# Kernel optimization log

Measured on AMD Instinct MI355X. Metric: run time of the kernel, lower is better.

## Reference

```python
import jax, jax.numpy as jnp
import numpy as np
import math

B, S, D, H = 8, 1024, 256, 8
HD = D // H  # head size = 32


def setup_inputs() -> dict:
    key = jax.random.key(0)
    ks = jax.random.split(key, 12)
    inp = {
        "query": jax.random.normal(ks[0], (B, S, D), jnp.float32),
        "key": jax.random.normal(ks[1], (B, S, D), jnp.float32),
        "value": jax.random.normal(ks[2], (B, S, D), jnp.float32),
        "rel": jax.random.uniform(ks[3], (B, S, S), jnp.float32),
        "timestamp": jax.random.normal(ks[4], (B, S, S), jnp.float32),
        "l1": jax.random.uniform(ks[5], (1,), jnp.float32),
        "l2": jax.random.uniform(ks[6], (1,), jnp.float32),
        # projection weights (nn.Linear: y = x @ W.T + b)
        "Wq": jax.random.normal(ks[7], (D, D), jnp.float32) / math.sqrt(D),
        "bq": jnp.zeros((D,), jnp.float32),
        "Wk": jax.random.normal(ks[8], (D, D), jnp.float32) / math.sqrt(D),
        "bk": jnp.zeros((D,), jnp.float32),
        "Wv": jax.random.normal(ks[9], (D, D), jnp.float32) / math.sqrt(D),
        "bv": jnp.zeros((D,), jnp.float32),
    }
    return inp


def reference(query, key, value, rel, timestamp, l1, l2, Wq, bq, Wk, bk, Wv, bv):
    b, s, d = query.shape
    h, hd = H, HD

    def proj(x, W, bias):
        # [b,s,d] -> [b,h,s,hd]
        return (x @ W.T + bias).reshape(b, s, h, hd).transpose(0, 2, 1, 3)

    q = proj(query, Wq, bq)
    k = proj(key, Wk, bk)
    v = proj(value, Wv, bv)

    # causal future mask: True above the diagonal (future positions)
    mask = jnp.triu(jnp.ones((s, s), dtype=bool), k=1)[None, None]  # [1,1,s,s]

    # relation attention: rel * mask, zeros -> -10000, softmax
    relm = rel[:, None] * mask.astype(rel.dtype)  # broadcast over heads [b,1->h,s,s]
    rel_attn = jax.nn.softmax(jnp.where(relm == 0, jnp.float32(-10000.0), relm), axis=-1)

    # scaled dot-product scores with causal mask
    scores = jnp.einsum('bhqd,bhkd->bhqk', q, k) / math.sqrt(hd)
    scores = jnp.where(mask, jnp.float32(-1e9), scores)
    prob_attn = jax.nn.softmax(scores, axis=-1)

    # time-decay attention: exp(-|t|), masked to -inf (use -1e30 for grad safety)
    ts = jnp.where(mask, jnp.float32(-1e30), jnp.exp(-jnp.abs(timestamp[:, None])))
    time_attn = jax.nn.softmax(ts, axis=-1)

    # blend (time_include=True, qrelation_include=True)
    prob = (1.0 - l2) * prob_attn + l2 * time_attn
    prob = (1.0 - l1) * prob + l1 * rel_attn

    out = jnp.einsum('bhqk,bhkd->bhqd', prob, v)
    out = out.transpose(0, 2, 1, 3).reshape(b, s, d)
    return out
```

## Files before the change

### kernel.cpp

```cpp
#include <hip/hip_runtime.h>
#include <math.h>

constexpr int B = 8, S = 1024, D = 256, H = 8, HD = 32;

typedef __attribute__((ext_vector_type(8))) short bf16x8;
typedef __attribute__((ext_vector_type(16))) float f32x16;
typedef __attribute__((ext_vector_type(2)))  int  int2v;

__device__ __forceinline__ uint cvtpk(float a, float b) {
    uint r;
    asm("v_cvt_pk_bf16_f32 %0, %1, %2" : "=v"(r) : "v"(a), "v"(b));
    return r;
}
__device__ __forceinline__ float xswap32f(float v, int hi) {
    int2v t = __builtin_amdgcn_permlane32_swap(__float_as_int(v), __float_as_int(v), false, false);
    return __int_as_float(hi ? t[0] : t[1]);
}

__global__ __launch_bounds__(512, 4) void proj_mfma(
    const float* __restrict__ query, const float* __restrict__ key_,
    const float* __restrict__ value,
    const float* __restrict__ Wq, const float* __restrict__ Wk,
    const float* __restrict__ Wv,
    const float* __restrict__ bq, const float* __restrict__ bk,
    const float* __restrict__ bv, float qscale,
    ushort* __restrict__ qbuf, ushort* __restrict__ kbuf,
    ushort* __restrict__ vtbuf, float* __restrict__ cpart)
{
    __shared__ ushort xf[8192];
    __shared__ float bias_lds[256];

    const int m = blockIdx.y;
    const int tid = threadIdx.x;
    const int w = tid >> 6, lane = tid & 63;
    const int l31 = lane & 31, hi = lane >> 5;
    const int h = w;

    const float* xsrc = (m == 0) ? query : (m == 1) ? key_ : value;
    const float* Wsrc = (m == 0) ? Wq : (m == 1) ? Wk : Wv;
    const float* bsrc = (m == 0) ? bq : (m == 1) ? bk : bv;
    ushort* yb = (m == 0) ? qbuf : (m == 1) ? kbuf : vtbuf;
    const float wscale = (m == 0) ? qscale : 1.0f;

    if (tid < 256) bias_lds[tid] = bsrc[tid] * wscale;

    bf16x8 wf[16];
    {
        const float* wrow = Wsrc + ((size_t)(h * 32 + l31)) * 256 + hi * 8;
        #pragma unroll
        for (int kc = 0; kc < 16; ++kc) {
            float4 a = *(const float4*)(wrow + kc * 16);
            float4 b = *(const float4*)(wrow + kc * 16 + 4);
            uint4 p;
            p.x = cvtpk(a.x * wscale, a.y * wscale);
            p.y = cvtpk(a.z * wscale, a.w * wscale);
            p.z = cvtpk(b.x * wscale, b.y * wscale);
            p.w = cvtpk(b.z * wscale, b.w * wscale);
            wf[kc] = __builtin_bit_cast(bf16x8, p);
        }
    }

    const int sst = tid & 31, skc = tid >> 5;
    float cpacc = 0.f;

    for (int it = 0; it < 2; ++it) {
        const int stile = blockIdx.x * 2 + it;
        const int b_ = stile >> 5, t32 = stile & 31;

        __syncthreads();
        {
            const float* xrow = xsrc + ((size_t)(stile * 32 + sst)) * 256 + skc * 16;
            float4 a0 = *(const float4*)(xrow + 0);
            float4 a1 = *(const float4*)(xrow + 4);
            float4 a2 = *(const float4*)(xrow + 8);
            float4 a3 = *(const float4*)(xrow + 12);
            uint2 w01 = { cvtpk(a0.x, a0.y), cvtpk(a0.z, a0.w) };
            uint2 w23 = { cvtpk(a1.x, a1.y), cvtpk(a1.z, a1.w) };
            uint2 w45 = { cvtpk(a2.x, a2.y), cvtpk(a2.z, a2.w) };
            uint2 w67 = { cvtpk(a3.x, a3.y), cvtpk(a3.z, a3.w) };
            ushort* base = xf + skc * 512 + sst * 4;
            *(uint2*)(base +   0) = w01;
            *(uint2*)(base + 128) = w23;
            *(uint2*)(base + 256) = w45;
            *(uint2*)(base + 384) = w67;
        }
        __syncthreads();

        f32x16 acc;
        #pragma unroll
        for (int r = 0; r < 16; ++r) acc[r] = 0.f;
        #pragma unroll
        for (int kc = 0; kc < 16; ++kc) {
            const ushort* rb = xf + kc * 512 + hi * 256 + l31 * 4;
            uint2 lo = *(const uint2*)rb;
            uint2 hj = *(const uint2*)(rb + 128);
            uint4 xw = { lo.x, lo.y, hj.x, hj.y };
            bf16x8 xfrag = __builtin_bit_cast(bf16x8, xw);
            if (m < 2)
                acc = __builtin_amdgcn_mfma_f32_32x32x16_bf16(wf[kc], xfrag, acc, 0, 0, 0);
            else
                acc = __builtin_amdgcn_mfma_f32_32x32x16_bf16(xfrag, wf[kc], acc, 0, 0, 0);
        }

        if (m < 2) {
            #pragma unroll
            for (int r = 0; r < 16; ++r)
                acc[r] += bias_lds[h * 32 + (r & 3) + 8 * (r >> 2) + 4 * hi];
        } else {
            const float bl = bias_lds[h * 32 + l31];
            #pragma unroll
            for (int r = 0; r < 16; ++r) acc[r] += bl;
            float cp = 0.f;
            #pragma unroll
            for (int r = 0; r < 16; ++r) cp += acc[r];
            cp += __shfl_xor(cp, 32);
            cpacc += cp;
        }

        uint wa0 = cvtpk(acc[0], acc[1]),   wa1 = cvtpk(acc[2], acc[3]);
        uint wb0 = cvtpk(acc[4], acc[5]),   wb1 = cvtpk(acc[6], acc[7]);
        uint wa2 = cvtpk(acc[8], acc[9]),   wa3 = cvtpk(acc[10], acc[11]);
        uint wb2 = cvtpk(acc[12], acc[13]), wb3 = cvtpk(acc[14], acc[15]);
        int2v s0 = __builtin_amdgcn_permlane32_swap((int)wa0, (int)wb0, false, false);
        int2v s1 = __builtin_amdgcn_permlane32_swap((int)wa1, (int)wb1, false, false);
        int2v s2 = __builtin_amdgcn_permlane32_swap((int)wa2, (int)wb2, false, false);
        int2v s3 = __builtin_amdgcn_permlane32_swap((int)wa3, (int)wb3, false, false);
        uint4 p0 = { (uint)s0[0], (uint)s1[0], (uint)s0[1], (uint)s1[1] };
        uint4 p1 = { (uint)s2[0], (uint)s3[0], (uint)s2[1], (uint)s3[1] };
        ushort* dst = yb + (((size_t)b_ * H + h) * 32 + t32) * 1024 + hi * 256 + l31 * 8;
        *(uint4*)dst = p0;
        *(uint4*)(dst + 512) = p1;
    }
    if (m == 2 && hi == 0)
        cpart[blockIdx.x * D + h * 32 + l31] = cpacc;
}

__global__ __launch_bounds__(512, 4) void timerel_mfma(
    const float* __restrict__ ts, const float* __restrict__ rel,
    const ushort* __restrict__ vtb, const float* __restrict__ cpart,
    const float* __restrict__ l1p, const float* __restrict__ l2p,
    float* __restrict__ out)
{
    __shared__ ushort wlds[32][1032];
    __shared__ float nuni[32];

    const int b  = blockIdx.y;
    const int i0 = blockIdx.x * 32;
    const int w = threadIdx.x >> 6, lane = threadIdx.x & 63;
    const int l31 = lane & 31, hi = lane >> 5;
    const float l1 = l1p[0], l2 = l2p[0];

    for (int r = 0; r < 4; ++r) {
        const int row = w * 4 + r;
        const int i = i0 + row;
        const float* tsrow  = ts  + ((size_t)b * S + i) * S;
        const float* relrow = rel + ((size_t)b * S + i) * S;

        float wv[4][4];
        float stp = 0.f, srp = 0.f;
        #pragma unroll
        for (int q = 0; q < 4; ++q) {
            const int jb = q * 256 + lane * 4;
            if (q * 256 + 255 <= i) {
                float4 t4 = *(const float4*)(tsrow + jb);
                const float te[4] = { t4.x, t4.y, t4.z, t4.w };
                #pragma unroll
                for (int e = 0; e < 4; ++e) {
                    float v = __expf(__expf(-fabsf(te[e])));
                    stp += v; wv[q][e] = v;
                }
            } else if (q * 256 > i) {
                float4 r4 = *(const float4*)(relrow + jb);
                const float re[4] = { r4.x, r4.y, r4.z, r4.w };
                #pragma unroll
                for (int e = 0; e < 4; ++e) {
                    float v = (re[e] != 0.f) ? __expf(re[e]) : 0.f;
                    srp += v; wv[q][e] = v;
                }
            } else {
                float4 t4 = *(const float4*)(tsrow + jb);
                float4 r4 = *(const float4*)(relrow + jb);
                const float te[4] = { t4.x, t4.y, t4.z, t4.w };
                const float re[4] = { r4.x, r4.y, r4.z, r4.w };
                #pragma unroll
                for (int e = 0; e < 4; ++e) {
                    float v;
                    if (jb + e <= i) { v = __expf(__expf(-fabsf(te[e]))); stp += v; }
                    else             { v = (re[e] != 0.f) ? __expf(re[e]) : 0.f; srp += v; }
                    wv[q][e] = v;
                }
            }
        }
        #pragma unroll
        for (int off = 1; off < 64; off <<= 1) {
            stp += __shfl_xor(stp, off);
            srp += __shfl_xor(srp, off);
        }
        const float nt = (1.f - l1) * l2 / stp;
        const float nr = (srp > 0.5f) ? (l1 / srp) : 0.f;
        if (lane == 0) nuni[row] = (srp > 0.5f) ? 0.f : (l1 / (float)S);
        #pragma unroll
        for (int q = 0; q < 4; ++q) {
            const int jb = q * 256 + lane * 4;
            float a0 = wv[q][0] * ((jb     <= i) ? nt : nr);
            float a1 = wv[q][1] * ((jb + 1 <= i) ? nt : nr);
            float a2 = wv[q][2] * ((jb + 2 <= i) ? nt : nr);
            float a3 = wv[q][3] * ((jb + 3 <= i) ? nt : nr);
            uint2 pk; pk.x = cvtpk(a0, a1); pk.y = cvtpk(a2, a3);
            *(uint2*)&wlds[row][jb] = pk;
        }
    }
    __syncthreads();

    const ushort* vtbase = vtb + ((size_t)b * 8 + w) * 32768 + hi * 256 + l31 * 8;
    f32x16 acc;
    #pragma unroll
    for (int r = 0; r < 16; ++r) acc[r] = 0.f;
    #pragma unroll 4
    for (int ks = 0; ks < 64; ++ks) {
        bf16x8 afrag = *(const bf16x8*)&wlds[l31][ks * 16 + hi * 8];
        bf16x8 vf = *(const bf16x8*)(vtbase + (size_t)ks * 512);
        acc = __builtin_amdgcn_mfma_f32_32x32x16_bf16(afrag, vf, acc, 0, 0, 0);
    }

    const int d = w * 32 + l31;
    float cv = 0.f;
    if (i0 == S - 32) {
        #pragma unroll
        for (int p_ = 0; p_ < 16; ++p_)
            cv += cpart[(b * 16 + p_) * D + d];
    }
    float* obase = out + ((size_t)b * S + i0) * D + d;
    #pragma unroll
    for (int r = 0; r < 16; ++r) {
        const int row = (r & 3) + 8 * (r >> 2) + 4 * hi;
        obase[(size_t)row * D] = acc[r] + nuni[row] * cv;
    }
}

#define LOADKV(K0, K1, V0, V1, KT) do { \
    const ushort* kp_ = kbase + (size_t)(KT) * 1024; \
    const ushort* vp_ = vbase + (size_t)(KT) * 1024; \
    K0 = *(const bf16x8*)kp_;        K1 = *(const bf16x8*)(kp_ + 512); \
    V0 = *(const bf16x8*)vp_;        V1 = *(const bf16x8*)(vp_ + 512); \
} while (0)

#define TILE_COMPUTE(K0, K1, V0, V1, ISDIAG) do { \
    f32x16 stv; \
    _Pragma("unroll") for (int r = 0; r < 16; ++r) stv[r] = 0.f; \
    stv = __builtin_amdgcn_mfma_f32_32x32x16_bf16(K0, qf0, stv, 0, 0, 0); \
    stv = __builtin_amdgcn_mfma_f32_32x32x16_bf16(K1, qf1, stv, 0, 0, 0); \
    if (ISDIAG) { \
        _Pragma("unroll") for (int r = 0; r < 16; ++r) \
            if (((r & 3) + 8 * (r >> 2) + 4 * hi) > l31) stv[r] = -1e30f; \
    } \
    float p[16]; \
    _Pragma("unroll") for (int r = 0; r < 16; ++r) { p[r] = exp2f(stv[r]); lacc += p[r]; } \
    uint wa0 = cvtpk(p[0], p[1]),   wa1 = cvtpk(p[2], p[3]); \
    uint wb0 = cvtpk(p[4], p[5]),   wb1 = cvtpk(p[6], p[7]); \
    uint wa2 = cvtpk(p[8], p[9]),   wa3 = cvtpk(p[10], p[11]); \
    uint wb2 = cvtpk(p[12], p[13]), wb3 = cvtpk(p[14], p[15]); \
    int2v s0 = __builtin_amdgcn_permlane32_swap((int)wa0, (int)wb0, false, false); \
    int2v s1 = __builtin_amdgcn_permlane32_swap((int)wa1, (int)wb1, false, false); \
    int2v s2 = __builtin_amdgcn_permlane32_swap((int)wa2, (int)wb2, false, false); \
    int2v s3 = __builtin_amdgcn_permlane32_swap((int)wa3, (int)wb3, false, false); \
    uint4 pa0i = { (uint)s0[0], (uint)s1[0], (uint)s0[1], (uint)s1[1] }; \
    uint4 pa1i = { (uint)s2[0], (uint)s3[0], (uint)s2[1], (uint)s3[1] }; \
    bf16x8 pa0 = __builtin_bit_cast(bf16x8, pa0i); \
    bf16x8 pa1 = __builtin_bit_cast(bf16x8, pa1i); \
    ot = __builtin_amdgcn_mfma_f32_32x32x16_bf16(V0, pa0, ot, 0, 0, 0); \
    ot = __builtin_amdgcn_mfma_f32_32x32x16_bf16(V1, pa1, ot, 0, 0, 0); \
} while (0)

__global__ __launch_bounds__(512, 4) void flash_mfma(
    const ushort* __restrict__ qb, const ushort* __restrict__ kb,
    const ushort* __restrict__ vtb, const float* __restrict__ l1p,
    const float* __restrict__ l2p, float* __restrict__ out)
{
    __shared__ float mbuf[4][64][18];
    __shared__ float lds_t[4][32 * 33];
    const int id = blockIdx.x;
    const int halfg = id >> 8, rr_ = id & 255;
    const int qraw = rr_ >> 5;
    const int qblk = halfg ? (7 - qraw) : qraw;
    const int bh = (rr_ & 31) | (halfg << 5);
    const int b = bh >> 3, h = bh & 7;
    const int w = threadIdx.x >> 6, lane = threadIdx.x & 63;
    const int sub = w & 3, half = w >> 2;
    const int l31 = lane & 31, hi = lane >> 5;
    const int qt = qblk * 4 + sub;
    const float c_p = (1.f - l1p[0]) * (1.f - l2p[0]);

    const ushort* qp_ = qb + ((size_t)bh * 32 + qt) * 1024 + hi * 256 + l31 * 8;
    const bf16x8 qf0 = *(const bf16x8*)qp_;
    const bf16x8 qf1 = *(const bf16x8*)(qp_ + 512);
    const ushort* kbase = kb  + (size_t)bh * 32768 + hi * 256 + l31 * 8;
    const ushort* vbase = vtb + (size_t)bh * 32768 + hi * 256 + l31 * 8;

    f32x16 ot;
    #pragma unroll
    for (int r = 0; r < 16; ++r) ot[r] = 0.f;
    float lacc = 0.f;

    const int nlo = (qt + 1) >> 1;
    const int klo = half ? nlo : 0;
    const int khi = half ? qt : (nlo - 1);

    if (klo <= khi) {
        bf16x8 kA0, kA1, vA0, vA1, kB0, kB1, vB0, vB1;
        LOADKV(kA0, kA1, vA0, vA1, klo);
        int kt = klo;
        for (;;) {
            if (kt + 1 <= khi) LOADKV(kB0, kB1, vB0, vB1, kt + 1);
            TILE_COMPUTE(kA0, kA1, vA0, vA1, kt == qt);
            if (++kt > khi) break;
            if (kt + 1 <= khi) LOADKV(kA0, kA1, vA0, vA1, kt + 1);
            TILE_COMPUTE(kB0, kB1, vB0, vB1, kt == qt);
            if (++kt > khi) break;
        }
    }

    if (half == 1) {
        float* mb = &mbuf[sub][lane][0];
        #pragma unroll
        for (int r = 0; r < 16; r += 4)
            *(float4*)&mb[r] = make_float4(ot[r], ot[r+1], ot[r+2], ot[r+3]);
        mb[16] = lacc;
    }
    __syncthreads();

    if (half == 0) {
        const float* mb = &mbuf[sub][lane][0];
        #pragma unroll
        for (int r = 0; r < 16; ++r) ot[r] += mb[r];
        lacc += mb[16];
        const float lrun = lacc + xswap32f(lacc, hi);
        const float inv = c_p / lrun;
        float* lt = lds_t[sub];
        #pragma unroll
        for (int r = 0; r < 16; ++r) {
            const int d = (r & 3) + 8 * (r >> 2) + 4 * hi;
            lt[l31 * 33 + d] = ot[r] * inv;
        }
    }
    __syncthreads();
    if (half == 0) {
        const int q0w = qt * 32;
        const float* lt = lds_t[sub];
        #pragma unroll
        for (int rr = 0; rr < 4; ++rr) {
            const int ql = rr * 8 + (lane >> 3);
            const int d0 = (lane & 7) * 4;
            const float* lp = &lt[ql * 33 + d0];
            float* op = out + ((size_t)b * S + q0w + ql) * D + h * 32 + d0;
            float4 cur = *(const float4*)op;
            cur.x += lp[0]; cur.y += lp[1]; cur.z += lp[2]; cur.w += lp[3];
            *(float4*)op = cur;
        }
    }
}

extern "C" void kernel_launch(void* const* d_in, const int* in_sizes, int n_in,
                              void* d_out, int out_size, void* d_ws, size_t ws_size,
                              hipStream_t stream)
{
    (void)in_sizes; (void)n_in; (void)out_size; (void)ws_size;
    const float* query = (const float*)d_in[0];
    const float* key_  = (const float*)d_in[1];
    const float* value = (const float*)d_in[2];
    const float* rel   = (const float*)d_in[3];
    const float* tsp   = (const float*)d_in[4];
    const float* l1p   = (const float*)d_in[5];
    const float* l2p   = (const float*)d_in[6];
    const float* Wq    = (const float*)d_in[7];
    const float* bq    = (const float*)d_in[8];
    const float* Wk    = (const float*)d_in[9];
    const float* bk    = (const float*)d_in[10];
    const float* Wv    = (const float*)d_in[11];
    const float* bv    = (const float*)d_in[12];
    float* out = (float*)d_out;

    ushort* qbuf  = (ushort*)d_ws;
    ushort* kbuf  = (ushort*)((char*)d_ws + (4u  << 20));
    ushort* vtbuf = (ushort*)((char*)d_ws + (8u  << 20));
    float*  cpart = (float*)((char*)d_ws + (12u << 20));

    const float qscale = 1.4426950408889634f * 0.17677669529663687f;

    proj_mfma<<<dim3(128, 3), 512, 0, stream>>>(
        query, key_, value, Wq, Wk, Wv, bq, bk, bv, qscale,
        qbuf, kbuf, vtbuf, cpart);

    timerel_mfma<<<dim3(S / 32, B), 512, 0, stream>>>(
        tsp, rel, vtbuf, cpart, l1p, l2p, out);

    flash_mfma<<<512, 512, 0, stream>>>(qbuf, kbuf, vtbuf, l1p, l2p, out);
}
```

Measured before the change: 66.44 us.

## Swizzle LDS weight layout and process two rows per pass in timerel

New measurement: 64.44 us. 3.0% less time.

```diff
diff --git a/kernel.cpp b/kernel.cpp
--- a/kernel.cpp
+++ b/kernel.cpp
@@ -141,7 +141,7 @@
     const float* __restrict__ l1p, const float* __restrict__ l2p,
     float* __restrict__ out)
 {
-    __shared__ ushort wlds[32][1032];
+    __shared__ ushort wlds[64 * 512];
     __shared__ float nuni[32];
 
     const int b  = blockIdx.y;
@@ -150,64 +150,80 @@
     const int l31 = lane & 31, hi = lane >> 5;
     const float l1 = l1p[0], l2 = l2p[0];
 
-    for (int r = 0; r < 4; ++r) {
-        const int row = w * 4 + r;
-        const int i = i0 + row;
-        const float* tsrow  = ts  + ((size_t)b * S + i) * S;
-        const float* relrow = rel + ((size_t)b * S + i) * S;
-
-        float wv[4][4];
-        float stp = 0.f, srp = 0.f;
-        #pragma unroll
-        for (int q = 0; q < 4; ++q) {
-            const int jb = q * 256 + lane * 4;
-            if (q * 256 + 255 <= i) {
-                float4 t4 = *(const float4*)(tsrow + jb);
-                const float te[4] = { t4.x, t4.y, t4.z, t4.w };
-                #pragma unroll
-                for (int e = 0; e < 4; ++e) {
-                    float v = __expf(__expf(-fabsf(te[e])));
-                    stp += v; wv[q][e] = v;
-                }
-            } else if (q * 256 > i) {
-                float4 r4 = *(const float4*)(relrow + jb);
-                const float re[4] = { r4.x, r4.y, r4.z, r4.w };
-                #pragma unroll
-                for (int e = 0; e < 4; ++e) {
-                    float v = (re[e] != 0.f) ? __expf(re[e]) : 0.f;
-                    srp += v; wv[q][e] = v;
-                }
-            } else {
-                float4 t4 = *(const float4*)(tsrow + jb);
-                float4 r4 = *(const float4*)(relrow + jb);
-                const float te[4] = { t4.x, t4.y, t4.z, t4.w };
-                const float re[4] = { r4.x, r4.y, r4.z, r4.w };
-                #pragma unroll
-                for (int e = 0; e < 4; ++e) {
-                    float v;
-                    if (jb + e <= i) { v = __expf(__expf(-fabsf(te[e]))); stp += v; }
-                    else             { v = (re[e] != 0.f) ? __expf(re[e]) : 0.f; srp += v; }
-                    wv[q][e] = v;
+    const int hig_w = (lane >> 1) & 1, jh_w = lane & 1;
+    const int ksl_lo = lane >> 2;
+
+    for (int pp = 0; pp < 2; ++pp) {
+        float wv[2][4][4];
+        float stp[2] = { 0.f, 0.f }, srp[2] = { 0.f, 0.f };
+        #pragma unroll
+        for (int rr = 0; rr < 2; ++rr) {
+            const int row = w * 4 + pp * 2 + rr;
+            const int i = i0 + row;
+            const float* tsrow  = ts  + ((size_t)b * S + i) * S;
+            const float* relrow = rel + ((size_t)b * S + i) * S;
+            #pragma unroll
+            for (int seg = 0; seg < 4; ++seg) {
+                const int jb = seg * 256 + lane * 4;
+                if (seg * 256 + 255 <= i) {
+                    float4 t4 = *(const float4*)(tsrow + jb);
+                    const float te[4] = { t4.x, t4.y, t4.z, t4.w };
+                    #pragma unroll
+                    for (int e = 0; e < 4; ++e) {
+                        float v = __expf(__expf(-fabsf(te[e])));
+                        stp[rr] += v; wv[rr][seg][e] = v;
+                    }
+                } else if (seg * 256 > i) {
+                    float4 r4 = *(const float4*)(relrow + jb);
+                    const float re[4] = { r4.x, r4.y, r4.z, r4.w };
+                    #pragma unroll
+                    for (int e = 0; e < 4; ++e) {
+                        float v = (re[e] != 0.f) ? __expf(re[e]) : 0.f;
+                        srp[rr] += v; wv[rr][seg][e] = v;
+                    }
+                } else {
+                    float4 t4 = *(const float4*)(tsrow + jb);
+                    float4 r4 = *(const float4*)(relrow + jb);
+                    const float te[4] = { t4.x, t4.y, t4.z, t4.w };
+                    const float re[4] = { r4.x, r4.y, r4.z, r4.w };
+                    #pragma unroll
+                    for (int e = 0; e < 4; ++e) {
+                        float v;
+                        if (jb + e <= i) { v = __expf(__expf(-fabsf(te[e]))); stp[rr] += v; }
+                        else             { v = (re[e] != 0.f) ? __expf(re[e]) : 0.f; srp[rr] += v; }
+                        wv[rr][seg][e] = v;
+                    }
                 }
             }
         }
         #pragma unroll
         for (int off = 1; off < 64; off <<= 1) {
-            stp += __shfl_xor(stp, off);
-            srp += __shfl_xor(srp, off);
-        }
-        const float nt = (1.f - l1) * l2 / stp;
-        const float nr = (srp > 0.5f) ? (l1 / srp) : 0.f;
-        if (lane == 0) nuni[row] = (srp > 0.5f) ? 0.f : (l1 / (float)S);
-        #pragma unroll
-        for (int q = 0; q < 4; ++q) {
-            const int jb = q * 256 + lane * 4;
-            float a0 = wv[q][0] * ((jb     <= i) ? nt : nr);
-            float a1 = wv[q][1] * ((jb + 1 <= i) ? nt : nr);
-            float a2 = wv[q][2] * ((jb + 2 <= i) ? nt : nr);
-            float a3 = wv[q][3] * ((jb + 3 <= i) ? nt : nr);
-            uint2 pk; pk.x = cvtpk(a0, a1); pk.y = cvtpk(a2, a3);
-            *(uint2*)&wlds[row][jb] = pk;
+            stp[0] += __shfl_xor(stp[0], off);
+            srp[0] += __shfl_xor(srp[0], off);
+            stp[1] += __shfl_xor(stp[1], off);
+            srp[1] += __shfl_xor(srp[1], off);
+        }
+        #pragma unroll
+        for (int rr = 0; rr < 2; ++rr) {
+            const int row = w * 4 + pp * 2 + rr;
+            const int i = i0 + row;
+            const float nt = (1.f - l1) * l2 / stp[rr];
+            const float nr = (srp[rr] > 0.5f) ? (l1 / srp[rr]) : 0.f;
+            if (lane == 0) nuni[row] = (srp[rr] > 0.5f) ? 0.f : (l1 / (float)S);
+            #pragma unroll
+            for (int seg = 0; seg < 4; ++seg) {
+                const int jb = seg * 256 + lane * 4;
+                float a0 = wv[rr][seg][0] * ((jb     <= i) ? nt : nr);
+                float a1 = wv[rr][seg][1] * ((jb + 1 <= i) ? nt : nr);
+                float a2 = wv[rr][seg][2] * ((jb + 2 <= i) ? nt : nr);
+                float a3 = wv[rr][seg][3] * ((jb + 3 <= i) ? nt : nr);
+                uint2 pk; pk.x = cvtpk(a0, a1); pk.y = cvtpk(a2, a3);
+                const int ksl = seg * 16 + ksl_lo;
+                const int xorv = jh_w | (hig_w << 1) | ((ksl & 7) << 2);
+                char* dst = (char*)wlds + ksl * 1024 + hig_w * 512 + jh_w * 256
+                            + ((row ^ xorv) & 31) * 8;
+                *(uint2*)dst = pk;
+            }
         }
     }
     __syncthreads();
@@ -218,7 +234,13 @@
     for (int r = 0; r < 16; ++r) acc[r] = 0.f;
     #pragma unroll 4
     for (int ks = 0; ks < 64; ++ks) {
-        bf16x8 afrag = *(const bf16x8*)&wlds[l31][ks * 16 + hi * 8];
+        const int x0 = 0 | (hi << 1) | ((ks & 7) << 2);
+        const int x1 = 1 | (hi << 1) | ((ks & 7) << 2);
+        const char* base = (const char*)wlds + ks * 1024 + hi * 512;
+        uint2 lo = *(const uint2*)(base +       ((l31 ^ x0) & 31) * 8);
+        uint2 hj = *(const uint2*)(base + 256 + ((l31 ^ x1) & 31) * 8);
+        uint4 aw = { lo.x, lo.y, hj.x, hj.y };
+        bf16x8 afrag = __builtin_bit_cast(bf16x8, aw);
         bf16x8 vf = *(const bf16x8*)(vtbase + (size_t)ks * 512);
         acc = __builtin_amdgcn_mfma_f32_32x32x16_bf16(afrag, vf, acc, 0, 0, 0);
     }
```
